# Optimization experiments

Measured on AMD Instinct MI355X. Metric: run time of the kernel, lower is better.

The kernel has to match this reference:

```python
import jax, jax.numpy as jnp
import numpy as np

N_EMBD = 768
N_HEAD = 12
HEAD_DIM = N_EMBD // N_HEAD


def setup_inputs() -> dict:
    key = jax.random.key(0)
    k0, k1, k2, k3, k4 = jax.random.split(key, 5)
    B, T, C = 2, 4096, N_EMBD
    x = jax.random.normal(k0, (B, T, C), dtype=jnp.float32)
    # c_attn: Linear(C, 3C); c_proj: Linear(C, C). torch Linear: y = x @ W.T + b
    s = 1.0 / np.sqrt(C)
    W_attn = jax.random.uniform(k1, (3 * C, C), dtype=jnp.float32, minval=-s, maxval=s)
    b_attn = jax.random.uniform(k2, (3 * C,), dtype=jnp.float32, minval=-s, maxval=s)
    W_proj = jax.random.uniform(k3, (C, C), dtype=jnp.float32, minval=-s, maxval=s)
    b_proj = jax.random.uniform(k4, (C,), dtype=jnp.float32, minval=-s, maxval=s)
    return {"x": x, "W_attn": W_attn, "b_attn": b_attn, "W_proj": W_proj, "b_proj": b_proj}


def reference(x, W_attn, b_attn, W_proj, b_proj):
    B, T, C = x.shape
    H, D = N_HEAD, HEAD_DIM
    qkv = x @ W_attn.T + b_attn                      # [B,T,3C]
    q, k, v = jnp.split(qkv, 3, axis=-1)
    # [B,T,C] -> [B,H,T,D]
    q = q.reshape(B, T, H, D).transpose(0, 2, 1, 3)
    k = k.reshape(B, T, H, D).transpose(0, 2, 1, 3)
    v = v.reshape(B, T, H, D).transpose(0, 2, 1, 3)
    scale = 1.0 / jnp.sqrt(jnp.asarray(D, dtype=x.dtype))
    att = jnp.einsum('bhqd,bhkd->bhqk', q, k) * scale  # [B,H,T,T]
    att = jax.nn.softmax(att, axis=-1)
    y = jnp.einsum('bhqk,bhkd->bhqd', att, v)          # [B,H,T,D]
    y = y.transpose(0, 2, 1, 3).reshape(B, T, C)
    return y @ W_proj.T + b_proj
```

## Files before the change

kernel.cpp:

```cpp
#include <hip/hip_runtime.h>
#include <stdint.h>
#include <stddef.h>

typedef __bf16 bf16_t;
typedef bf16_t bf16x4 __attribute__((ext_vector_type(4)));
typedef bf16_t bf16x8 __attribute__((ext_vector_type(8)));
typedef float  f32x4  __attribute__((ext_vector_type(4)));
typedef _Float16 f16_t;
typedef f16_t f16x4 __attribute__((ext_vector_type(4)));

#define MFMA_BF16_K32(a, b, c) __builtin_amdgcn_mfma_f32_16x16x32_bf16(a, b, c, 0, 0, 0)
#define MFMA_F16_K16(a, b, c)  __builtin_amdgcn_mfma_f32_16x16x16f16(a, b, c, 0, 0, 0)

__device__ __forceinline__ void gload_lds16(const void* g, void* l) {
    __builtin_amdgcn_global_load_lds(
        (const __attribute__((address_space(1))) void*)g,
        (__attribute__((address_space(3))) void*)l,
        16, 0, 0);
}

#define NX 1572864
#define NWA 442368
#define NWP 147456
__global__ void cvt_all(const float* __restrict__ x, const float* __restrict__ Wa,
                        const float* __restrict__ Wp, bf16_t* __restrict__ xb,
                        bf16_t* __restrict__ Wab, bf16_t* __restrict__ Wpb) {
    int i = blockIdx.x * blockDim.x + threadIdx.x;
    const float4* src; bf16_t* dst; int j;
    if (i < NX)            { src = (const float4*)x;  dst = xb;  j = i; }
    else if (i < NX + NWA) { src = (const float4*)Wa; dst = Wab; j = i - NX; }
    else                   { src = (const float4*)Wp; dst = Wpb; j = i - NX - NWA; }
    float4 f = src[j];
    bf16x4 o = { (bf16_t)f.x, (bf16_t)f.y, (bf16_t)f.z, (bf16_t)f.w };
    ((bf16x4*)dst)[j] = o;
}

template <int KDIM>
__device__ __forceinline__ void gemm_mainloop(
    const bf16_t* __restrict__ A, const bf16_t* __restrict__ Bt,
    bf16_t* As, bf16_t* Bs, int m0, int n0, int wave, int lane, f32x4 acc[4][4])
{
    const int quad = lane >> 4, l15 = lane & 15;
    const int wm = ((wave >> 1) << 6), wn = ((wave & 1) << 6);

    const int srow = (wave << 4) + (lane >> 2);
    const int sw   = (((lane & 3) ^ ((srow >> 1) & 3)) << 3);
    const bf16_t* gA = A  + (size_t)(m0 + srow) * KDIM + sw;
    const bf16_t* gB = Bt + (size_t)(n0 + srow) * KDIM + sw;
    bf16_t* lA0 = As + wave * 512;
    bf16_t* lA1 = As + 2048 + wave * 512;
    bf16_t* lB0 = Bs + wave * 512;
    bf16_t* lB1 = Bs + 2048 + wave * 512;

    const int xorv = ((quad ^ ((l15 >> 1) & 3)) << 3);

    for (int k0 = 0; k0 < KDIM; k0 += 32) {
        __syncthreads();
        gload_lds16(gA + k0,                       lA0);
        gload_lds16(gA + (size_t)64 * KDIM + k0,   lA1);
        gload_lds16(gB + k0,                       lB0);
        gload_lds16(gB + (size_t)64 * KDIM + k0,   lB1);
        __syncthreads();

        bf16x8 af[4], bfr[4];
#pragma unroll
        for (int t = 0; t < 4; t++) {
            af[t]  = *(const bf16x8*)(As + (wm + t * 16 + l15) * 32 + xorv);
            bfr[t] = *(const bf16x8*)(Bs + (wn + t * 16 + l15) * 32 + xorv);
        }
#pragma unroll
        for (int mt = 0; mt < 4; mt++)
#pragma unroll
            for (int nt = 0; nt < 4; nt++)
                acc[mt][nt] = MFMA_BF16_K32(af[mt], bfr[nt], acc[mt][nt]);
    }
}

__global__ __launch_bounds__(256) void gemm_qkv(
    const bf16_t* __restrict__ A,
    const bf16_t* __restrict__ Bt,
    const float* __restrict__ bias,
    bf16_t* __restrict__ qo, bf16_t* __restrict__ ko, f16_t* __restrict__ vo)
{
    __shared__ bf16_t As[128 * 32];
    __shared__ bf16_t Bs[128 * 32];
    const int tid = threadIdx.x, wave = tid >> 6, lane = tid & 63;
    const int quad = lane >> 4, l15 = lane & 15;
    const int m0 = blockIdx.y * 128, n0 = blockIdx.x * 128;
    f32x4 acc[4][4] = {};
    gemm_mainloop<768>(A, Bt, As, Bs, m0, n0, wave, lane, acc);

    const int wm = ((wave >> 1) << 6), wn = ((wave & 1) << 6);
#pragma unroll
    for (int nt = 0; nt < 4; nt++) {
        const int cc = n0 + wn + nt * 16 + l15;
        const float bia = bias[cc];
        const int which = cc / 768;
        const int rem = cc - which * 768;
        const int h = rem >> 6, d = rem & 63;
        if (which < 2) {
            bf16_t* dst = (which == 0) ? qo : ko;
#pragma unroll
            for (int mt = 0; mt < 4; mt++) {
#pragma unroll
                for (int r = 0; r < 4; r++) {
                    const int row = m0 + wm + mt * 16 + quad * 4 + r;
                    const int b = row >> 12, t = row & 4095;
                    dst[((size_t)(b * 12 + h) * 4096 + t) * 64 + d] =
                        (bf16_t)(acc[mt][nt][r] + bia);
                }
            }
        } else {
#pragma unroll
            for (int mt = 0; mt < 4; mt++) {
                const int row0 = m0 + wm + mt * 16 + quad * 4;
                const int b = row0 >> 12, t0 = row0 & 4095;
                f16x4 ov = { (f16_t)(acc[mt][nt][0] + bia),
                             (f16_t)(acc[mt][nt][1] + bia),
                             (f16_t)(acc[mt][nt][2] + bia),
                             (f16_t)(acc[mt][nt][3] + bia) };
                *(f16x4*)(vo + ((size_t)(b * 12 + h) * 64 + d) * 4096 + t0) = ov;
            }
        }
    }
}

__global__ __launch_bounds__(256) void gemm_proj(
    const bf16_t* __restrict__ A,
    const bf16_t* __restrict__ Bt,
    const float* __restrict__ bias,
    float* __restrict__ out)
{
    __shared__ bf16_t As[128 * 32];
    __shared__ bf16_t Bs[128 * 32];
    const int tid = threadIdx.x, wave = tid >> 6, lane = tid & 63;
    const int quad = lane >> 4, l15 = lane & 15;
    const int m0 = blockIdx.y * 128, n0 = blockIdx.x * 128;
    f32x4 acc[4][4] = {};
    gemm_mainloop<768>(A, Bt, As, Bs, m0, n0, wave, lane, acc);

    const int wm = ((wave >> 1) << 6), wn = ((wave & 1) << 6);
#pragma unroll
    for (int nt = 0; nt < 4; nt++) {
        const int cc = n0 + wn + nt * 16 + l15;
        const float bia = bias[cc];
#pragma unroll
        for (int mt = 0; mt < 4; mt++) {
#pragma unroll
            for (int r = 0; r < 4; r++) {
                const int row = m0 + wm + mt * 16 + quad * 4 + r;
                out[(size_t)row * 768 + cc] = acc[mt][nt][r] + bia;
            }
        }
    }
}

#define QSCALE 0.1803368801f
__global__ __launch_bounds__(256, 3) void attn_fwd(
    const bf16_t* __restrict__ qg, const bf16_t* __restrict__ kg,
    const f16_t* __restrict__ vtg, bf16_t* __restrict__ y)
{
    __shared__ bf16_t Ks0[64 * 64], Ks1[64 * 64];
    __shared__ f16_t  Vt0[64 * 64], Vt1[64 * 64];
    const int tid = threadIdx.x, wave = tid >> 6, lane = tid & 63;
    const int quad = lane >> 4, l15 = lane & 15;
    const int qt = blockIdx.x, bh = blockIdx.y;
    const int b = bh / 12, h = bh - b * 12;
    const size_t base = (size_t)bh * 4096 * 64;
    const bf16_t* kgt = kg + base;
    const f16_t*  vgt = vtg + base;

    bf16x8 qf[2][2];
#pragma unroll
    for (int rt = 0; rt < 2; rt++) {
        const int qrow = qt * 128 + wave * 32 + rt * 16 + l15;
        qf[rt][0] = *(const bf16x8*)(qg + base + (size_t)qrow * 64 + quad * 8);
        qf[rt][1] = *(const bf16x8*)(qg + base + (size_t)qrow * 64 + 32 + quad * 8);
#pragma unroll
        for (int j = 0; j < 8; j++) {
            qf[rt][0][j] = (bf16_t)((float)qf[rt][0][j] * QSCALE);
            qf[rt][1][j] = (bf16_t)((float)qf[rt][1][j] * QSCALE);
        }
    }

    const f16_t onef = (f16_t)1.0f;
    const f16x4 onesf = { onef, onef, onef, onef };

    f32x4 O[2][4] = {};
    f32x4 Osum[2] = {};

    const int srow8 = tid >> 3;
    const int sc8   = (tid & 7) ^ (srow8 & 7);
    const int ksoff = (quad ^ (l15 & 7)) << 3;
    const int l8 = l15 & 7, q1 = quad >> 1, q0off = (quad & 1) * 8;

    auto stage = [&](int kt, bf16_t* Kd, f16_t* Vd) {
        const bf16_t* kp = kgt + (size_t)kt * 64 * 64;
        const f16_t*  vp = vgt + kt * 64;
#pragma unroll
        for (int i = 0; i < 2; i++) {
            gload_lds16(kp + (i * 32 + srow8) * 64 + sc8 * 8,           Kd + (i * 256 + tid) * 8);
            gload_lds16(vp + (size_t)(i * 32 + srow8) * 4096 + sc8 * 8, Vd + (i * 256 + tid) * 8);
        }
    };

    auto compute = [&](const bf16_t* ks, const f16_t* vs) {
        f32x4 sc[2][4];
#pragma unroll
        for (int ct = 0; ct < 4; ct++) {
            const bf16_t* kr = ks + (ct * 16 + l15) * 64;
            bf16x8 kf0 = *(const bf16x8*)(kr + ksoff);
            bf16x8 kf1 = *(const bf16x8*)(kr + (ksoff ^ 32));
            f32x4 s0 = {}, s1 = {};
            s0 = MFMA_BF16_K32(kf0, qf[0][0], s0);
            s0 = MFMA_BF16_K32(kf1, qf[0][1], s0);
            s1 = MFMA_BF16_K32(kf0, qf[1][0], s1);
            s1 = MFMA_BF16_K32(kf1, qf[1][1], s1);
            sc[0][ct] = s0; sc[1][ct] = s1;
        }
        f16x4 pf[2][4];
#pragma unroll
        for (int rt = 0; rt < 2; rt++)
#pragma unroll
            for (int ct = 0; ct < 4; ct++) {
                f16x4 p = { (f16_t)exp2f(sc[rt][ct][0]), (f16_t)exp2f(sc[rt][ct][1]),
                            (f16_t)exp2f(sc[rt][ct][2]), (f16_t)exp2f(sc[rt][ct][3]) };
                pf[rt][ct] = p;
            }
#pragma unroll
        for (int dt = 0; dt < 4; dt++) {
            const char* vr = (const char*)(vs + (dt * 16 + l15) * 64);
#pragma unroll
            for (int kk = 0; kk < 4; kk++) {
                const int slot = ((kk << 1) | q1) ^ l8;
                f16x4 vf = *(const f16x4*)(vr + slot * 16 + q0off);
                O[0][dt] = MFMA_F16_K16(vf, pf[0][kk], O[0][dt]);
                O[1][dt] = MFMA_F16_K16(vf, pf[1][kk], O[1][dt]);
            }
        }
#pragma unroll
        for (int rt = 0; rt < 2; rt++)
#pragma unroll
            for (int kk = 0; kk < 4; kk++)
                Osum[rt] = MFMA_F16_K16(onesf, pf[rt][kk], Osum[rt]);
    };

    stage(0, Ks0, Vt0);
    for (int kt = 0; kt < 64; kt += 2) {
        __syncthreads();
        stage(kt + 1, Ks1, Vt1);
        compute(Ks0, Vt0);
        __syncthreads();
        if (kt + 2 < 64) stage(kt + 2, Ks0, Vt0);
        compute(Ks1, Vt1);
    }

#pragma unroll
    for (int rt = 0; rt < 2; rt++) {
        const float rcp = 1.0f / Osum[rt][0];
        const int t = qt * 128 + wave * 32 + rt * 16 + l15;
        bf16_t* yr = y + ((size_t)b * 4096 + t) * 768 + h * 64 + quad * 4;
#pragma unroll
        for (int dt = 0; dt < 4; dt++) {
            bf16x4 ov = { (bf16_t)(O[rt][dt][0] * rcp), (bf16_t)(O[rt][dt][1] * rcp),
                          (bf16_t)(O[rt][dt][2] * rcp), (bf16_t)(O[rt][dt][3] * rcp) };
            *(bf16x4*)(yr + dt * 16) = ov;
        }
    }
}

extern "C" void kernel_launch(void* const* d_in, const int* in_sizes, int n_in,
                              void* d_out, int out_size, void* d_ws, size_t ws_size,
                              hipStream_t stream) {
    const float* x  = (const float*)d_in[0];
    const float* Wa = (const float*)d_in[1];
    const float* ba = (const float*)d_in[2];
    const float* Wp = (const float*)d_in[3];
    const float* bp = (const float*)d_in[4];
    float* out = (float*)d_out;

    char* ws = (char*)d_ws;
    bf16_t* xb  = (bf16_t*)(ws);
    bf16_t* Wab = (bf16_t*)(ws + 12582912);
    bf16_t* Wpb = (bf16_t*)(ws + 16121856);
    bf16_t* qb  = (bf16_t*)(ws + 17301504);
    bf16_t* kb  = (bf16_t*)(ws + 29884416);
    f16_t*  vtb = (f16_t*)(ws + 42467328);
    bf16_t* yb  = (bf16_t*)(ws + 55050240);

    cvt_all<<<8448, 256, 0, stream>>>(x, Wa, Wp, xb, Wab, Wpb);
    gemm_qkv <<<dim3(18, 64), 256, 0, stream>>>(xb, Wab, ba, qb, kb, vtb);
    attn_fwd <<<dim3(32, 24), 256, 0, stream>>>(qb, kb, vtb, yb);
    gemm_proj<<<dim3( 6, 64), 256, 0, stream>>>(yb, Wpb, bp, out);
}
```

Before: 313.2 us.

## Halve attention query tile, XCD-aware block mapping, scalar row-sum instead of MFMA

Measured after the change: 329.5 us. 1.05x slower.

```diff
diff --git a/kernel.cpp b/kernel.cpp
--- a/kernel.cpp
+++ b/kernel.cpp
@@ -156,7 +156,7 @@
 }
 
 #define QSCALE 0.1803368801f
-__global__ __launch_bounds__(256, 3) void attn_fwd(
+__global__ __launch_bounds__(256, 5) void attn_fwd(
     const bf16_t* __restrict__ qg, const bf16_t* __restrict__ kg,
     const f16_t* __restrict__ vtg, bf16_t* __restrict__ y)
 {
@@ -164,30 +164,30 @@
     __shared__ f16_t  Vt0[64 * 64], Vt1[64 * 64];
     const int tid = threadIdx.x, wave = tid >> 6, lane = tid & 63;
     const int quad = lane >> 4, l15 = lane & 15;
-    const int qt = blockIdx.x, bh = blockIdx.y;
+
+    const int blk = blockIdx.x;
+    const int xcd = blk & 7;
+    const int idx = blk >> 3;
+    const int hl  = idx % 3;
+    const int qt  = idx / 3;
+    const int bh  = xcd * 3 + hl;
     const int b = bh / 12, h = bh - b * 12;
     const size_t base = (size_t)bh * 4096 * 64;
     const bf16_t* kgt = kg + base;
     const f16_t*  vgt = vtg + base;
 
-    bf16x8 qf[2][2];
-#pragma unroll
-    for (int rt = 0; rt < 2; rt++) {
-        const int qrow = qt * 128 + wave * 32 + rt * 16 + l15;
-        qf[rt][0] = *(const bf16x8*)(qg + base + (size_t)qrow * 64 + quad * 8);
-        qf[rt][1] = *(const bf16x8*)(qg + base + (size_t)qrow * 64 + 32 + quad * 8);
-#pragma unroll
-        for (int j = 0; j < 8; j++) {
-            qf[rt][0][j] = (bf16_t)((float)qf[rt][0][j] * QSCALE);
-            qf[rt][1][j] = (bf16_t)((float)qf[rt][1][j] * QSCALE);
-        }
-    }
-
-    const f16_t onef = (f16_t)1.0f;
-    const f16x4 onesf = { onef, onef, onef, onef };
-
-    f32x4 O[2][4] = {};
-    f32x4 Osum[2] = {};
+    const int qrow = qt * 64 + wave * 16 + l15;
+    bf16x8 qf[2];
+    qf[0] = *(const bf16x8*)(qg + base + (size_t)qrow * 64 + quad * 8);
+    qf[1] = *(const bf16x8*)(qg + base + (size_t)qrow * 64 + 32 + quad * 8);
+#pragma unroll
+    for (int j = 0; j < 8; j++) {
+        qf[0][j] = (bf16_t)((float)qf[0][j] * QSCALE);
+        qf[1][j] = (bf16_t)((float)qf[1][j] * QSCALE);
+    }
+
+    f32x4 O[4] = {};
+    float psum = 0.f;
 
     const int srow8 = tid >> 3;
     const int sc8   = (tid & 7) ^ (srow8 & 7);
@@ -205,28 +205,26 @@
     };
 
     auto compute = [&](const bf16_t* ks, const f16_t* vs) {
-        f32x4 sc[2][4];
+        f32x4 sc[4];
 #pragma unroll
         for (int ct = 0; ct < 4; ct++) {
             const bf16_t* kr = ks + (ct * 16 + l15) * 64;
             bf16x8 kf0 = *(const bf16x8*)(kr + ksoff);
             bf16x8 kf1 = *(const bf16x8*)(kr + (ksoff ^ 32));
-            f32x4 s0 = {}, s1 = {};
-            s0 = MFMA_BF16_K32(kf0, qf[0][0], s0);
-            s0 = MFMA_BF16_K32(kf1, qf[0][1], s0);
-            s1 = MFMA_BF16_K32(kf0, qf[1][0], s1);
-            s1 = MFMA_BF16_K32(kf1, qf[1][1], s1);
-            sc[0][ct] = s0; sc[1][ct] = s1;
-        }
-        f16x4 pf[2][4];
-#pragma unroll
-        for (int rt = 0; rt < 2; rt++)
-#pragma unroll
-            for (int ct = 0; ct < 4; ct++) {
-                f16x4 p = { (f16_t)exp2f(sc[rt][ct][0]), (f16_t)exp2f(sc[rt][ct][1]),
-                            (f16_t)exp2f(sc[rt][ct][2]), (f16_t)exp2f(sc[rt][ct][3]) };
-                pf[rt][ct] = p;
-            }
+            f32x4 s = {};
+            s = MFMA_BF16_K32(kf0, qf[0], s);
+            s = MFMA_BF16_K32(kf1, qf[1], s);
+            sc[ct] = s;
+        }
+        f16x4 pf[4];
+#pragma unroll
+        for (int ct = 0; ct < 4; ct++) {
+            float e0 = exp2f(sc[ct][0]), e1 = exp2f(sc[ct][1]);
+            float e2 = exp2f(sc[ct][2]), e3 = exp2f(sc[ct][3]);
+            psum += (e0 + e1) + (e2 + e3);
+            f16x4 p = { (f16_t)e0, (f16_t)e1, (f16_t)e2, (f16_t)e3 };
+            pf[ct] = p;
+        }
 #pragma unroll
         for (int dt = 0; dt < 4; dt++) {
             const char* vr = (const char*)(vs + (dt * 16 + l15) * 64);
@@ -234,15 +232,9 @@
             for (int kk = 0; kk < 4; kk++) {
                 const int slot = ((kk << 1) | q1) ^ l8;
                 f16x4 vf = *(const f16x4*)(vr + slot * 16 + q0off);
-                O[0][dt] = MFMA_F16_K16(vf, pf[0][kk], O[0][dt]);
-                O[1][dt] = MFMA_F16_K16(vf, pf[1][kk], O[1][dt]);
-            }
-        }
-#pragma unroll
-        for (int rt = 0; rt < 2; rt++)
-#pragma unroll
-            for (int kk = 0; kk < 4; kk++)
-                Osum[rt] = MFMA_F16_K16(onesf, pf[rt][kk], Osum[rt]);
+                O[dt] = MFMA_F16_K16(vf, pf[kk], O[dt]);
+            }
+        }
     };
 
     stage(0, Ks0, Vt0);
@@ -255,17 +247,16 @@
         compute(Ks1, Vt1);
     }
 
-#pragma unroll
-    for (int rt = 0; rt < 2; rt++) {
-        const float rcp = 1.0f / Osum[rt][0];
-        const int t = qt * 128 + wave * 32 + rt * 16 + l15;
-        bf16_t* yr = y + ((size_t)b * 4096 + t) * 768 + h * 64 + quad * 4;
-#pragma unroll
-        for (int dt = 0; dt < 4; dt++) {
-            bf16x4 ov = { (bf16_t)(O[rt][dt][0] * rcp), (bf16_t)(O[rt][dt][1] * rcp),
-                          (bf16_t)(O[rt][dt][2] * rcp), (bf16_t)(O[rt][dt][3] * rcp) };
-            *(bf16x4*)(yr + dt * 16) = ov;
-        }
+    psum += __shfl_xor(psum, 16, 64);
+    psum += __shfl_xor(psum, 32, 64);
+    const float rcp = 1.0f / psum;
+    const int t = qt * 64 + wave * 16 + l15;
+    bf16_t* yr = y + ((size_t)b * 4096 + t) * 768 + h * 64 + quad * 4;
+#pragma unroll
+    for (int dt = 0; dt < 4; dt++) {
+        bf16x4 ov = { (bf16_t)(O[dt][0] * rcp), (bf16_t)(O[dt][1] * rcp),
+                      (bf16_t)(O[dt][2] * rcp), (bf16_t)(O[dt][3] * rcp) };
+        *(bf16x4*)(yr + dt * 16) = ov;
     }
 }
 
@@ -290,6 +281,6 @@
 
     cvt_all<<<8448, 256, 0, stream>>>(x, Wa, Wp, xb, Wab, Wpb);
     gemm_qkv <<<dim3(18, 64), 256, 0, stream>>>(xb, Wab, ba, qb, kb, vtb);
-    attn_fwd <<<dim3(32, 24), 256, 0, stream>>>(qb, kb, vtb, yb);
+    attn_fwd <<<1536, 256, 0, stream>>>(qb, kb, vtb, yb);
     gemm_proj<<<dim3( 6, 64), 256, 0, stream>>>(yb, Wpb, bp, out);
 }
```
